# Kernel optimization log

Hardware: AMD Instinct MI355X
Metric: run time of the kernel (lower is better)

The kernel has to match this reference:

```python
import jax, jax.numpy as jnp
import numpy as np

TOP_K = 2  # num_experts_per_tok


def setup_inputs() -> dict:
    key = jax.random.key(0)
    k1, k2, k3, k4, k5 = jax.random.split(key, 5)
    T, H, F, E = 2048, 2048, 1024, 8
    hidden_states = jax.random.normal(k1, (T, H), dtype=jnp.float32)
    router_logits = jax.random.normal(k2, (T, E), dtype=jnp.float32)
    s = 1.0 / np.sqrt(H)
    w1 = jax.random.normal(k3, (E, H, F), dtype=jnp.float32) * s  # gate proj
    w3 = jax.random.normal(k4, (E, H, F), dtype=jnp.float32) * s  # up proj
    w2 = jax.random.normal(k5, (E, F, H), dtype=jnp.float32) * (1.0 / np.sqrt(F))  # down proj
    return {"hidden_states": hidden_states, "router_logits": router_logits,
            "w1": w1, "w3": w3, "w2": w2}


def reference(hidden_states, router_logits, w1, w3, w2):
    # Top-K routing: softmax over raw logits, take top-k probs as combine weights
    # (renormalize_topk_logits=False, routed_scaling_factor=None).
    T, E = router_logits.shape
    probs = jax.nn.softmax(router_logits.astype(jnp.float32), axis=-1)  # (T, E)
    topk_w, topk_ids = jax.lax.top_k(probs, TOP_K)                      # (T, K)
    # Scatter combine weights into a dense (T, E) matrix (zeros off top-k).
    combine = jnp.zeros((T, E), dtype=probs.dtype).at[
        jnp.arange(T)[:, None], topk_ids].add(topk_w)                    # (T, E)

    x = hidden_states
    # SwiGLU expert FFN computed per-expert (dense over all tokens, masked by
    # combine weights -> same math as fused dispatch/grouped-GEMM/combine).
    g = jnp.einsum('th,ehf->etf', x, w1)          # (E, T, F) gate
    u = jnp.einsum('th,ehf->etf', x, w3)          # (E, T, F) up
    act = jax.nn.silu(g) * u                      # (E, T, F)
    act = act * combine.T[:, :, None]             # apply combine weight pre-down-proj
    y = jnp.einsum('etf,efh->th', act, w2)        # (T, H) combined over experts
    return y.astype(hidden_states.dtype)
```

## Files before the change

kernel.cpp:

```cpp
#include <hip/hip_runtime.h>
#include <stdint.h>

#define T_TOK 2048
#define HDIM  2048
#define FDIM  1024
#define NEXP  8

#define BM   128
#define BK   64
#define NTHR 256
#define MT_MAX 16
#define BN1  64
#define BN2  128
#define NT1 (FDIM / BN1)
#define NT2 (HDIM / BN2)
#define NK1 (HDIM / BK)
#define NK2 (FDIM / BK)
#define GRID2K (NEXP * MT_MAX * NT2)
#define TILE_E 4096
#define SMEM_BYTES 36864

typedef unsigned short u16;
typedef __attribute__((ext_vector_type(16))) float f32x16;
typedef __attribute__((ext_vector_type(8))) short bf16x8;

__device__ __forceinline__ u16 f2bf(float f) {
  uint32_t u = __float_as_uint(f);
  u += 0x7FFFu + ((u >> 16) & 1u);
  return (u16)(u >> 16);
}

__device__ __forceinline__ uint32_t pack2(float lo, float hi) {
  return (uint32_t)f2bf(lo) | ((uint32_t)f2bf(hi) << 16);
}

__device__ __forceinline__ void glds16(const u16* src, u16* dst) {
  __builtin_amdgcn_global_load_lds(
      (const __attribute__((address_space(1))) uint32_t*)src,
      (__attribute__((address_space(3))) uint32_t*)dst, 16, 0, 0);
}

__global__ void route1_kernel(const float* __restrict__ logits,
                              int* __restrict__ tok_e, float* __restrict__ tok_w,
                              int* __restrict__ counts) {
  __shared__ int lcnt[NEXP];
  const int tid = threadIdx.x;
  const int t = blockIdx.x * 256 + tid;
  if (tid < NEXP) lcnt[tid] = 0;
  __syncthreads();
  float l[NEXP];
#pragma unroll
  for (int e = 0; e < NEXP; ++e) l[e] = logits[t * NEXP + e];
  float m = l[0];
#pragma unroll
  for (int e = 1; e < NEXP; ++e) m = fmaxf(m, l[e]);
  float p[NEXP]; float s = 0.f;
#pragma unroll
  for (int e = 0; e < NEXP; ++e) { p[e] = __expf(l[e] - m); s += p[e]; }
  float inv = 1.f / s;
  int i0 = 0; float p0 = p[0];
#pragma unroll
  for (int e = 1; e < NEXP; ++e) if (p[e] > p0) { p0 = p[e]; i0 = e; }
  int i1 = -1; float p1 = -1.f;
#pragma unroll
  for (int e = 0; e < NEXP; ++e) if (e != i0 && p[e] > p1) { p1 = p[e]; i1 = e; }
  tok_e[t] = i0 | (i1 << 8);
  tok_w[t * 2]     = p0 * inv;
  tok_w[t * 2 + 1] = p1 * inv;
  atomicAdd(&lcnt[i0], 1);
  atomicAdd(&lcnt[i1], 1);
  __syncthreads();
  if (tid < NEXP) atomicAdd(&counts[tid], lcnt[tid]);
}

__global__ void route2_kernel(const int* __restrict__ counts,
                              int* __restrict__ offsets, int* __restrict__ cursor) {
  if (threadIdx.x == 0) {
    int s = 0;
    for (int e = 0; e < NEXP; ++e) { offsets[e] = s; cursor[e] = s; s += counts[e]; }
    offsets[NEXP] = s;
  }
}

__global__ void route3_kernel(const int* __restrict__ tok_e, const float* __restrict__ tok_w,
                              int* __restrict__ cursor,
                              int* __restrict__ token_list, float* __restrict__ slot_w) {
  __shared__ int lcnt[NEXP], lbase[NEXP];
  const int tid = threadIdx.x;
  const int t = blockIdx.x * 256 + tid;
  if (tid < NEXP) lcnt[tid] = 0;
  __syncthreads();
  int ee = tok_e[t];
  int e0 = ee & 255, e1 = ee >> 8;
  int li0 = atomicAdd(&lcnt[e0], 1);
  int li1 = atomicAdd(&lcnt[e1], 1);
  __syncthreads();
  if (tid < NEXP) lbase[tid] = atomicAdd(&cursor[tid], lcnt[tid]);
  __syncthreads();
  int s0 = lbase[e0] + li0;
  int s1 = lbase[e1] + li1;
  token_list[s0] = t; slot_w[s0] = tok_w[t * 2];
  token_list[s1] = t; slot_w[s1] = tok_w[t * 2 + 1];
}

__device__ __forceinline__ void wconv2_block(const float* __restrict__ src,
                                             u16* __restrict__ dstb,
                                             int C, int NT, int NKT,
                                             int e, int kt, int cb, uint32_t* U) {
  const int t = threadIdx.x;
  {
    const int n = t & 127;
    const int half = t >> 7;
    const float* col0 = src + (size_t)(kt * 64 + half * 32) * C + cb * 128 + n;
    uint32_t pk[16];
#pragma unroll
    for (int q = 0; q < 16; ++q) {
      float a = col0[(size_t)(2 * q) * C];
      float b = col0[(size_t)(2 * q + 1) * C];
      pk[q] = pack2(a, b);
    }
    uint32_t* d = &U[n * 33 + half * 16];
#pragma unroll
    for (int q4 = 0; q4 < 4; ++q4)
      *(uint4*)(d + q4 * 4) = make_uint4(pk[q4 * 4], pk[q4 * 4 + 1], pk[q4 * 4 + 2], pk[q4 * 4 + 3]);
  }
  __syncthreads();
  {
    const int ct2 = t >> 7;
    const int jj = t & 127;
    const int nn = jj >> 1;
    const int hb = jj & 1;
    const int s = (nn >> 2) & 1;
    const int gct = cb * 2 + ct2;
    u16* tb = dstb + (((size_t)e * NT + gct) * NKT + kt) * TILE_E + nn * 16 + ((hb ^ s) * 8);
    const uint32_t* up = &U[(ct2 * 64 + nn) * 33 + hb * 4];
#pragma unroll
    for (int kq = 0; kq < 4; ++kq) {
      uint4 v = *(const uint4*)(up + kq * 8);
      *(uint4*)(tb + kq * 1024) = v;
    }
  }
}

__global__ __launch_bounds__(256, 4)
void mega1_kernel(const float* __restrict__ w1, const float* __restrict__ w3,
                  u16* __restrict__ w1b, u16* __restrict__ w3b,
                  const float4* __restrict__ x, ushort4* __restrict__ xb,
                  float4* __restrict__ y4) {
  __shared__ __align__(16) uint32_t U[128 * 33];
  const int bid = blockIdx.x;
  const int t = threadIdx.x;
  if (bid < 4096) {
    const int m = bid >> 11;
    const int r = bid & 2047;
    const int e = r >> 8;
    const int rr = r & 255;
    const int kt = rr >> 3;
    const int cb = rr & 7;
    const size_t msz = (size_t)HDIM * FDIM;
    wconv2_block((m ? w3 : w1) + (size_t)e * msz, m ? w3b : w1b,
                 FDIM, 16, 32, e, kt, cb, U);
  } else if (bid < 4352) {
    int i = (bid - 4096) * 256 + t;
#pragma unroll
    for (int r = 0; r < 16; ++r, i += 65536) {
      float4 v = x[i];
      ushort4 o;
      o.x = f2bf(v.x); o.y = f2bf(v.y); o.z = f2bf(v.z); o.w = f2bf(v.w);
      xb[i] = o;
    }
  } else {
    int i = (bid - 4352) * 256 + t;
    float4 z = {0.f, 0.f, 0.f, 0.f};
#pragma unroll
    for (int r = 0; r < 16; ++r, i += 65536) y4[i] = z;
  }
}

__global__ __launch_bounds__(256, 3)
void mega2_kernel(const float* __restrict__ w2, u16* __restrict__ w2b,
                  const u16* __restrict__ Xb,
                  const u16* __restrict__ w1b, const u16* __restrict__ w3b,
                  const int* __restrict__ token_list,
                  const float* __restrict__ slot_w,
                  const int* __restrict__ counts,
                  const int* __restrict__ offsets,
                  u16* __restrict__ act) {
  __shared__ __align__(16) uint8_t smem[SMEM_BYTES];
  const int bid = blockIdx.x;
  if (bid >= 2048) {
    const int r = bid - 2048;
    const int e = r >> 8;
    const int rr = r & 255;
    const int kt = rr >> 4;
    const int cb = rr & 15;
    wconv2_block(w2 + (size_t)e * HDIM * FDIM, w2b,
                 HDIM, 32, 16, e, kt, cb, (uint32_t*)smem);
    return;
  }
  const int gb = bid;
  const int e  = gb >> 8;
  const int mt = (gb >> 4) & 15;
  const int nt = gb & 15;
  const int cnt = counts[e];
  if (mt * BM >= cnt) return;
  const int off = offsets[e];
  const int tid  = threadIdx.x;
  const int lane = tid & 63;
  const int wid  = tid >> 6;
  const int wr = wid >> 1;
  const int wc = wid & 1;

  u16* A_lds  = (u16*)smem;
  u16* B1_lds = (u16*)(smem + 16384);
  u16* B3_lds = (u16*)(smem + 24576);

  const u16* a_src[4];
#pragma unroll
  for (int i = 0; i < 4; ++i) {
    int row = (wid * 4 + i) * 8 + (lane >> 3);
    int mg = mt * BM + row;
    int mc = (mg < cnt) ? mg : (cnt - 1);
    int tok = token_list[off + mc];
    a_src[i] = Xb + (size_t)tok * HDIM + (((lane & 7) ^ (row & 7)) * 8);
  }
  const u16* b1_src[2];
  const u16* b3_src[2];
  {
    size_t tbase = ((size_t)(e * 16 + nt) * 32) * TILE_E;
#pragma unroll
    for (int i = 0; i < 2; ++i) {
      int c = wid * 2 + i;
      b1_src[i] = w1b + tbase + c * 512 + lane * 8;
      b3_src[i] = w3b + tbase + c * 512 + lane * 8;
    }
  }

  f32x16 accg[2] = {};
  f32x16 accu[2] = {};

#pragma unroll
  for (int i = 0; i < 4; ++i) glds16(a_src[i], &A_lds[(wid * 4 + i) * 512]);
#pragma unroll
  for (int i = 0; i < 2; ++i) {
    glds16(b1_src[i], &B1_lds[(wid * 2 + i) * 512]);
    glds16(b3_src[i], &B3_lds[(wid * 2 + i) * 512]);
  }

#pragma unroll 1
  for (int t = 0; t < NK1; ++t) {
    __syncthreads();
    bf16x8 af[2][4], bg[4], bu[4];
#pragma unroll
    for (int m = 0; m < 2; ++m) {
      int R = wr * 64 + m * 32 + (lane & 31);
#pragma unroll
      for (int kk = 0; kk < 4; ++kk) {
        int gl = kk * 2 + (lane >> 5);
        af[m][kk] = *(const bf16x8*)&A_lds[R * BK + ((gl ^ (R & 7)) * 8)];
      }
    }
    {
      int R = wc * 32 + (lane & 31);
      int base = R * 16 + (((lane >> 5) ^ ((R >> 2) & 1)) * 8);
#pragma unroll
      for (int kk = 0; kk < 4; ++kk) {
        bg[kk] = *(const bf16x8*)&B1_lds[base + kk * 1024];
        bu[kk] = *(const bf16x8*)&B3_lds[base + kk * 1024];
      }
    }
    __syncthreads();
    if (t + 1 < NK1) {
      const size_t ks = (size_t)(t + 1) * BK;
      const size_t kb = (size_t)(t + 1) * TILE_E;
#pragma unroll
      for (int i = 0; i < 4; ++i) glds16(a_src[i] + ks, &A_lds[(wid * 4 + i) * 512]);
#pragma unroll
      for (int i = 0; i < 2; ++i) {
        glds16(b1_src[i] + kb, &B1_lds[(wid * 2 + i) * 512]);
        glds16(b3_src[i] + kb, &B3_lds[(wid * 2 + i) * 512]);
      }
    }
#pragma unroll
    for (int m = 0; m < 2; ++m)
#pragma unroll
      for (int kk = 0; kk < 4; ++kk) {
        accg[m] = __builtin_amdgcn_mfma_f32_32x32x16_bf16(af[m][kk], bg[kk], accg[m], 0, 0, 0);
        accu[m] = __builtin_amdgcn_mfma_f32_32x32x16_bf16(af[m][kk], bu[kk], accu[m], 0, 0, 0);
      }
  }

  const int fcol = nt * BN1 + wc * 32 + (lane & 31);
#pragma unroll
  for (int m = 0; m < 2; ++m) {
    int base = mt * BM + wr * 64 + m * 32 + 4 * (lane >> 5);
#pragma unroll
    for (int reg = 0; reg < 16; ++reg) {
      int mg = base + (reg & 3) + 8 * (reg >> 2);
      if (mg < cnt) {
        int slot = off + mg;
        float wgt = slot_w[slot];
        float g = accg[m][reg];
        float u = accu[m][reg];
        float sv = g / (1.f + __expf(-g));
        act[(size_t)slot * FDIM + fcol] = f2bf(sv * u * wgt);
      }
    }
  }
}

__global__ __launch_bounds__(NTHR, 3)
void gemm2_kernel(const u16* __restrict__ act,
                  const u16* __restrict__ w2b,
                  const int* __restrict__ token_list,
                  const int* __restrict__ counts,
                  const int* __restrict__ offsets,
                  float* __restrict__ y) {
  const int bid = blockIdx.x;
  const int e  = bid >> 8;
  const int mt = (bid >> 4) & 15;
  const int nt = bid & 15;
  const int cnt = counts[e];
  if (mt * BM >= cnt) return;
  const int off = offsets[e];
  const int tid  = threadIdx.x;
  const int lane = tid & 63;
  const int wid  = tid >> 6;
  const int wr = wid >> 1;
  const int wc = wid & 1;

  __shared__ u16 A_lds[BM * BK];
  __shared__ u16 B_lds[BN2 * BK];

  const u16* a_src[4];
  const u16* b_src[4];
#pragma unroll
  for (int i = 0; i < 4; ++i) {
    int row = (wid * 4 + i) * 8 + (lane >> 3);
    int mg = mt * BM + row;
    int mc = (mg < cnt) ? mg : (cnt - 1);
    a_src[i] = act + (size_t)(off + mc) * FDIM + (((lane & 7) ^ (row & 7)) * 8);
    int c = wid * 4 + i;
    size_t tbase = ((size_t)(e * 32 + nt * 2 + (c >> 3)) * 16) * TILE_E;
    b_src[i] = w2b + tbase + (c & 7) * 512 + lane * 8;
  }

  f32x16 acc[2][2] = {};

#pragma unroll
  for (int i = 0; i < 4; ++i) {
    glds16(a_src[i], &A_lds[(wid * 4 + i) * 512]);
    glds16(b_src[i], &B_lds[(wid * 4 + i) * 512]);
  }

#pragma unroll 1
  for (int t = 0; t < NK2; ++t) {
    __syncthreads();
    bf16x8 af[2][4], bb[2][4];
#pragma unroll
    for (int m = 0; m < 2; ++m) {
      int R = wr * 64 + m * 32 + (lane & 31);
#pragma unroll
      for (int kk = 0; kk < 4; ++kk) {
        int gl = kk * 2 + (lane >> 5);
        af[m][kk] = *(const bf16x8*)&A_lds[R * BK + ((gl ^ (R & 7)) * 8)];
      }
    }
#pragma unroll
    for (int n = 0; n < 2; ++n) {
      int R = wc * 64 + n * 32 + (lane & 31);
      int base = (R >> 6) * TILE_E + (R & 63) * 16 + (((lane >> 5) ^ ((R >> 2) & 1)) * 8);
#pragma unroll
      for (int kk = 0; kk < 4; ++kk)
        bb[n][kk] = *(const bf16x8*)&B_lds[base + kk * 1024];
    }
    __syncthreads();
    if (t + 1 < NK2) {
      const size_t ks = (size_t)(t + 1) * BK;
      const size_t kb = (size_t)(t + 1) * TILE_E;
#pragma unroll
      for (int i = 0; i < 4; ++i) {
        glds16(a_src[i] + ks, &A_lds[(wid * 4 + i) * 512]);
        glds16(b_src[i] + kb, &B_lds[(wid * 4 + i) * 512]);
      }
    }
#pragma unroll
    for (int kk = 0; kk < 4; ++kk)
#pragma unroll
      for (int m = 0; m < 2; ++m)
#pragma unroll
        for (int n = 0; n < 2; ++n)
          acc[m][n] = __builtin_amdgcn_mfma_f32_32x32x16_bf16(af[m][kk], bb[n][kk], acc[m][n], 0, 0, 0);
  }

#pragma unroll
  for (int m = 0; m < 2; ++m) {
    int base = mt * BM + wr * 64 + m * 32 + 4 * (lane >> 5);
#pragma unroll
    for (int reg = 0; reg < 16; ++reg) {
      int mg = base + (reg & 3) + 8 * (reg >> 2);
      if (mg < cnt) {
        int slot = off + mg;
        int tok = token_list[slot];
#pragma unroll
        for (int n = 0; n < 2; ++n) {
          int hcol = nt * BN2 + wc * 64 + n * 32 + (lane & 31);
          unsafeAtomicAdd(y + (size_t)tok * HDIM + hcol, acc[m][n][reg]);
        }
      }
    }
  }
}

extern "C" void kernel_launch(void* const* d_in, const int* in_sizes, int n_in,
                              void* d_out, int out_size, void* d_ws, size_t ws_size,
                              hipStream_t stream) {
  (void)in_sizes; (void)n_in; (void)out_size; (void)ws_size;
  const float* hs     = (const float*)d_in[0];
  const float* logits = (const float*)d_in[1];
  const float* w1     = (const float*)d_in[2];
  const float* w3     = (const float*)d_in[3];
  const float* w2     = (const float*)d_in[4];
  float* y = (float*)d_out;

  uint8_t* ws = (uint8_t*)d_ws;
  int*   token_list = (int*)(ws);
  float* slot_w     = (float*)(ws + (16 << 10));
  int*   counts     = (int*)(ws + (32 << 10));
  int*   offsets    = (int*)(ws + (32 << 10) + 128);
  int*   cursor     = (int*)(ws + (32 << 10) + 256);
  int*   tok_e      = (int*)(ws + (33 << 10));
  float* tok_w      = (float*)(ws + (42 << 10));
  const size_t MB = 1 << 20;
  u16*   Xb  = (u16*)(ws + (64 << 10));
  u16*   act = (u16*)(ws + (64 << 10) + 8 * MB);
  u16*   w1b = (u16*)(ws + (64 << 10) + 16 * MB);
  u16*   w3b = (u16*)(ws + (64 << 10) + 48 * MB);
  u16*   w2b = (u16*)(ws + (64 << 10) + 80 * MB);

  hipMemsetAsync(counts, 0, NEXP * sizeof(int), stream);
  route1_kernel<<<T_TOK / 256, 256, 0, stream>>>(logits, tok_e, tok_w, counts);
  route2_kernel<<<1, 64, 0, stream>>>(counts, offsets, cursor);
  route3_kernel<<<T_TOK / 256, 256, 0, stream>>>(tok_e, tok_w, cursor, token_list, slot_w);
  mega1_kernel<<<4608, 256, 0, stream>>>(w1, w3, w1b, w3b,
                                         (const float4*)hs, (ushort4*)Xb, (float4*)y);
  mega2_kernel<<<4096, 256, 0, stream>>>(w2, w2b, Xb, w1b, w3b,
                                         token_list, slot_w, counts, offsets, act);
  gemm2_kernel<<<GRID2K, NTHR, 0, stream>>>(act, w2b, token_list, counts, offsets, y);
}
```

Baseline: 163.9 us.

## Split weight conversion across kernels to overlap with per-expert gate/up GEMM

```diff
diff --git a/kernel.cpp b/kernel.cpp
--- a/kernel.cpp
+++ b/kernel.cpp
@@ -142,66 +142,16 @@
   }
 }
 
-__global__ __launch_bounds__(256, 4)
-void mega1_kernel(const float* __restrict__ w1, const float* __restrict__ w3,
-                  u16* __restrict__ w1b, u16* __restrict__ w3b,
-                  const float4* __restrict__ x, ushort4* __restrict__ xb,
-                  float4* __restrict__ y4) {
-  __shared__ __align__(16) uint32_t U[128 * 33];
-  const int bid = blockIdx.x;
-  const int t = threadIdx.x;
-  if (bid < 4096) {
-    const int m = bid >> 11;
-    const int r = bid & 2047;
-    const int e = r >> 8;
-    const int rr = r & 255;
-    const int kt = rr >> 3;
-    const int cb = rr & 7;
-    const size_t msz = (size_t)HDIM * FDIM;
-    wconv2_block((m ? w3 : w1) + (size_t)e * msz, m ? w3b : w1b,
-                 FDIM, 16, 32, e, kt, cb, U);
-  } else if (bid < 4352) {
-    int i = (bid - 4096) * 256 + t;
-#pragma unroll
-    for (int r = 0; r < 16; ++r, i += 65536) {
-      float4 v = x[i];
-      ushort4 o;
-      o.x = f2bf(v.x); o.y = f2bf(v.y); o.z = f2bf(v.z); o.w = f2bf(v.w);
-      xb[i] = o;
-    }
-  } else {
-    int i = (bid - 4352) * 256 + t;
-    float4 z = {0.f, 0.f, 0.f, 0.f};
-#pragma unroll
-    for (int r = 0; r < 16; ++r, i += 65536) y4[i] = z;
-  }
-}
-
-__global__ __launch_bounds__(256, 3)
-void mega2_kernel(const float* __restrict__ w2, u16* __restrict__ w2b,
-                  const u16* __restrict__ Xb,
-                  const u16* __restrict__ w1b, const u16* __restrict__ w3b,
-                  const int* __restrict__ token_list,
-                  const float* __restrict__ slot_w,
-                  const int* __restrict__ counts,
-                  const int* __restrict__ offsets,
-                  u16* __restrict__ act) {
-  __shared__ __align__(16) uint8_t smem[SMEM_BYTES];
-  const int bid = blockIdx.x;
-  if (bid >= 2048) {
-    const int r = bid - 2048;
-    const int e = r >> 8;
-    const int rr = r & 255;
-    const int kt = rr >> 4;
-    const int cb = rr & 15;
-    wconv2_block(w2 + (size_t)e * HDIM * FDIM, w2b,
-                 HDIM, 32, 16, e, kt, cb, (uint32_t*)smem);
-    return;
-  }
-  const int gb = bid;
-  const int e  = gb >> 8;
-  const int mt = (gb >> 4) & 15;
-  const int nt = gb & 15;
+__device__ __forceinline__ void gemm1_body(int e, int mt, int nt,
+                                           const u16* __restrict__ Xb,
+                                           const u16* __restrict__ w1b,
+                                           const u16* __restrict__ w3b,
+                                           const int* __restrict__ token_list,
+                                           const float* __restrict__ slot_w,
+                                           const int* __restrict__ counts,
+                                           const int* __restrict__ offsets,
+                                           u16* __restrict__ act,
+                                           uint8_t* smem) {
   const int cnt = counts[e];
   if (mt * BM >= cnt) return;
   const int off = offsets[e];
@@ -307,6 +257,94 @@
       }
     }
   }
+}
+
+__global__ __launch_bounds__(256, 4)
+void mega1a_kernel(const float* __restrict__ w1, const float* __restrict__ w3,
+                   u16* __restrict__ w1b, u16* __restrict__ w3b,
+                   const float4* __restrict__ x, ushort4* __restrict__ xb,
+                   float4* __restrict__ y4) {
+  __shared__ __align__(16) uint32_t U[128 * 33];
+  const int bid = blockIdx.x;
+  const int t = threadIdx.x;
+  if (bid < 2048) {
+    const int m = bid >> 10;
+    const int r = bid & 1023;
+    const int e = r >> 8;
+    const int rr = r & 255;
+    const int kt = rr >> 3;
+    const int cb = rr & 7;
+    const size_t msz = (size_t)HDIM * FDIM;
+    wconv2_block((m ? w3 : w1) + (size_t)e * msz, m ? w3b : w1b,
+                 FDIM, 16, 32, e, kt, cb, U);
+  } else if (bid < 2304) {
+    int i = (bid - 2048) * 256 + t;
+#pragma unroll
+    for (int r = 0; r < 16; ++r, i += 65536) {
+      float4 v = x[i];
+      ushort4 o;
+      o.x = f2bf(v.x); o.y = f2bf(v.y); o.z = f2bf(v.z); o.w = f2bf(v.w);
+      xb[i] = o;
+    }
+  } else {
+    int i = (bid - 2304) * 256 + t;
+    float4 z = {0.f, 0.f, 0.f, 0.f};
+#pragma unroll
+    for (int r = 0; r < 16; ++r, i += 65536) y4[i] = z;
+  }
+}
+
+__global__ __launch_bounds__(256, 3)
+void mega2a_kernel(const float* __restrict__ w1, const float* __restrict__ w3,
+                   u16* __restrict__ w1b, u16* __restrict__ w3b,
+                   const u16* __restrict__ Xb,
+                   const int* __restrict__ token_list,
+                   const float* __restrict__ slot_w,
+                   const int* __restrict__ counts,
+                   const int* __restrict__ offsets,
+                   u16* __restrict__ act) {
+  __shared__ __align__(16) uint8_t smem[SMEM_BYTES];
+  const int bid = blockIdx.x;
+  if (bid >= 1024) {
+    const int r = bid - 1024;
+    const int m = r >> 10;
+    const int r1 = r & 1023;
+    const int e = 4 + (r1 >> 8);
+    const int rr = r1 & 255;
+    const int kt = rr >> 3;
+    const int cb = rr & 7;
+    const size_t msz = (size_t)HDIM * FDIM;
+    wconv2_block((m ? w3 : w1) + (size_t)e * msz, m ? w3b : w1b,
+                 FDIM, 16, 32, e, kt, cb, (uint32_t*)smem);
+    return;
+  }
+  gemm1_body(bid >> 8, (bid >> 4) & 15, bid & 15,
+             Xb, w1b, w3b, token_list, slot_w, counts, offsets, act, smem);
+}
+
+__global__ __launch_bounds__(256, 3)
+void mega2b_kernel(const float* __restrict__ w2, u16* __restrict__ w2b,
+                   const u16* __restrict__ Xb,
+                   const u16* __restrict__ w1b, const u16* __restrict__ w3b,
+                   const int* __restrict__ token_list,
+                   const float* __restrict__ slot_w,
+                   const int* __restrict__ counts,
+                   const int* __restrict__ offsets,
+                   u16* __restrict__ act) {
+  __shared__ __align__(16) uint8_t smem[SMEM_BYTES];
+  const int bid = blockIdx.x;
+  if (bid >= 1024) {
+    const int r = bid - 1024;
+    const int e = r >> 8;
+    const int rr = r & 255;
+    const int kt = rr >> 4;
+    const int cb = rr & 15;
+    wconv2_block(w2 + (size_t)e * HDIM * FDIM, w2b,
+                 HDIM, 32, 16, e, kt, cb, (uint32_t*)smem);
+    return;
+  }
+  gemm1_body(4 + (bid >> 8), (bid >> 4) & 15, bid & 15,
+             Xb, w1b, w3b, token_list, slot_w, counts, offsets, act, smem);
 }
 
 __global__ __launch_bounds__(NTHR, 3)
@@ -442,9 +480,11 @@
   route1_kernel<<<T_TOK / 256, 256, 0, stream>>>(logits, tok_e, tok_w, counts);
   route2_kernel<<<1, 64, 0, stream>>>(counts, offsets, cursor);
   route3_kernel<<<T_TOK / 256, 256, 0, stream>>>(tok_e, tok_w, cursor, token_list, slot_w);
-  mega1_kernel<<<4608, 256, 0, stream>>>(w1, w3, w1b, w3b,
-                                         (const float4*)hs, (ushort4*)Xb, (float4*)y);
-  mega2_kernel<<<4096, 256, 0, stream>>>(w2, w2b, Xb, w1b, w3b,
-                                         token_list, slot_w, counts, offsets, act);
+  mega1a_kernel<<<2560, 256, 0, stream>>>(w1, w3, w1b, w3b,
+                                          (const float4*)hs, (ushort4*)Xb, (float4*)y);
+  mega2a_kernel<<<3072, 256, 0, stream>>>(w1, w3, w1b, w3b, Xb,
+                                          token_list, slot_w, counts, offsets, act);
+  mega2b_kernel<<<3072, 256, 0, stream>>>(w2, w2b, Xb, w1b, w3b,
+                                          token_list, slot_w, counts, offsets, act);
   gemm2_kernel<<<GRID2K, NTHR, 0, stream>>>(act, w2b, token_list, counts, offsets, y);
 }
```

Result: slower. 199.4 us (+21.7%).
